# Kernel tuning notes

Measured on AMD Instinct MI355X. Metric: run time of the kernel, lower is better.

Reference implementation:

```python
import jax, jax.numpy as jnp
import numpy as np

DIM = 320
HEADS = 8
D_HEAD = 40
CTX_DIM = 768
INNER_FF = 4 * DIM  # 1280
EPS = 1e-5


def _ln(x, w, b):
    mu = jnp.mean(x, axis=-1, keepdims=True)
    var = jnp.mean(jnp.square(x - mu), axis=-1, keepdims=True)
    return (x - mu) * jax.lax.rsqrt(var + EPS) * w + b


def _attn(xq, ctx, Wq, Wk, Wv, Wo, bo):
    # Wq: [dim, inner]; Wk/Wv: [ctx_dim, inner]; Wo: [inner, dim]
    b, n, _ = xq.shape
    m = ctx.shape[1]
    scale = D_HEAD ** -0.5
    q = (xq @ Wq).reshape(b, n, HEADS, D_HEAD)
    k = (ctx @ Wk).reshape(b, m, HEADS, D_HEAD)
    v = (ctx @ Wv).reshape(b, m, HEADS, D_HEAD)
    sim = jnp.einsum('bihd,bjhd->bhij', q, k) * scale
    attn = jax.nn.softmax(sim, axis=-1)
    out = jnp.einsum('bhij,bjhd->bihd', attn, v).reshape(b, n, HEADS * D_HEAD)
    return out @ Wo + bo


def setup_inputs() -> dict:
    key = jax.random.key(0)
    ks = jax.random.split(key, 20)
    s = 0.02
    inner = HEADS * D_HEAD  # 320
    d = {
        'x': jax.random.normal(ks[0], (2, 4096, DIM), jnp.float32),
        'context': jax.random.normal(ks[1], (2, 77, CTX_DIM), jnp.float32),
        # norm params
        'ln1_w': jnp.ones((DIM,)), 'ln1_b': jnp.zeros((DIM,)),
        'ln2_w': jnp.ones((DIM,)), 'ln2_b': jnp.zeros((DIM,)),
        'ln3_w': jnp.ones((DIM,)), 'ln3_b': jnp.zeros((DIM,)),
        # attn1 (self)
        'a1_Wq': jax.random.normal(ks[2], (DIM, inner)) * s,
        'a1_Wk': jax.random.normal(ks[3], (DIM, inner)) * s,
        'a1_Wv': jax.random.normal(ks[4], (DIM, inner)) * s,
        'a1_Wo': jax.random.normal(ks[5], (inner, DIM)) * s,
        'a1_bo': jnp.zeros((DIM,)),
        # attn2 (cross)
        'a2_Wq': jax.random.normal(ks[6], (DIM, inner)) * s,
        'a2_Wk': jax.random.normal(ks[7], (CTX_DIM, inner)) * s,
        'a2_Wv': jax.random.normal(ks[8], (CTX_DIM, inner)) * s,
        'a2_Wo': jax.random.normal(ks[9], (inner, DIM)) * s,
        'a2_bo': jnp.zeros((DIM,)),
        # GEGLU feed-forward
        'ff_W1': jax.random.normal(ks[10], (DIM, 2 * INNER_FF)) * s,
        'ff_b1': jnp.zeros((2 * INNER_FF,)),
        'ff_W2': jax.random.normal(ks[11], (INNER_FF, DIM)) * s,
        'ff_b2': jnp.zeros((DIM,)),
    }
    return d


def reference(x, context, ln1_w, ln1_b, ln2_w, ln2_b, ln3_w, ln3_b,
              a1_Wq, a1_Wk, a1_Wv, a1_Wo, a1_bo,
              a2_Wq, a2_Wk, a2_Wv, a2_Wo, a2_bo,
              ff_W1, ff_b1, ff_W2, ff_b2):
    h = _ln(x, ln1_w, ln1_b)
    x = _attn(h, h, a1_Wq, a1_Wk, a1_Wv, a1_Wo, a1_bo) + x
    h = _ln(x, ln2_w, ln2_b)
    x = _attn(h, context, a2_Wq, a2_Wk, a2_Wv, a2_Wo, a2_bo) + x
    h = _ln(x, ln3_w, ln3_b)
    proj = h @ ff_W1 + ff_b1
    u, gate = jnp.split(proj, 2, axis=-1)
    ff = (u * jax.nn.gelu(gate, approximate=False)) @ ff_W2 + ff_b2
    return ff + x
```

## Files before the change

### kernel.cpp

```cpp
#include <hip/hip_runtime.h>
#include <hip/hip_bf16.h>
#include <math.h>

typedef __hip_bfloat16 bf16;
typedef __attribute__((ext_vector_type(8))) short bf16x8;
typedef __attribute__((ext_vector_type(4))) short bf16x4;
typedef __attribute__((ext_vector_type(4))) float f32x4;
typedef __attribute__((ext_vector_type(2))) unsigned int u32x2;

#define DIM 320
#define HEADS 8
#define DHEAD 40
#define CTXD 768
#define FFI 1280
#define NQ 4096
#define NCTX 77
#define BATCH 2

static __device__ __forceinline__ short f2bs(float v) {
    union { bf16 b; short s; } x; x.b = __float2bfloat16(v); return x.s;
}
static __device__ __forceinline__ float bs2f(short s) {
    return __uint_as_float(((unsigned)(unsigned short)s) << 16);
}
static __device__ __forceinline__ unsigned pkbf(float hi, float lo) {
    return __builtin_amdgcn_perm(__float_as_uint(hi), __float_as_uint(lo), 0x07060302u);
}

__global__ void __launch_bounds__(256) wtrans_all(
    const float* q1s, const float* k1s, const float* v1s, const float* o1s,
    const float* q2s, const float* o2s, const float* k2s, const float* v2s,
    const float* w1s, const float* w2s,
    short* q1d, short* k1d, short* v1d, short* o1d,
    short* q2d, short* o2d, short* k2d, short* v2d,
    short* w1d, short* w2d)
{
    int bid = blockIdx.x;
    const float* W; short* Wt; int K, N, base;
    if (bid < 600) {
        int ws = bid / 100; base = bid % 100; K = DIM; N = DIM;
        W  = ws == 0 ? q1s : ws == 1 ? k1s : ws == 2 ? v1s : ws == 3 ? o1s : ws == 4 ? q2s : o2s;
        Wt = ws == 0 ? q1d : ws == 1 ? k1d : ws == 2 ? v1d : ws == 3 ? o1d : ws == 4 ? q2d : o2d;
    } else if (bid < 1080) {
        int i = bid - 600; int ws = i / 240; base = i % 240; K = CTXD; N = DIM;
        W = ws ? v2s : k2s; Wt = ws ? v2d : k2d;
    } else if (bid < 1880) {
        base = bid - 1080; K = DIM; N = 2 * FFI; W = w1s; Wt = w1d;
    } else {
        base = bid - 1880; K = FFI; N = DIM; W = w2s; Wt = w2d;
    }
    int ntx = N / 32;
    int n0 = (base % ntx) * 32, k0 = (base / ntx) * 32;
    __shared__ float T[32][33];
    int c = threadIdx.x & 31, r8 = threadIdx.x >> 5;
#pragma unroll
    for (int rr = 0; rr < 4; ++rr) {
        int r = r8 + rr * 8;
        T[r][c] = W[(size_t)(k0 + r) * N + n0 + c];
    }
    __syncthreads();
#pragma unroll
    for (int rr = 0; rr < 4; ++rr) {
        int r = r8 + rr * 8;
        Wt[(size_t)(n0 + r) * K + k0 + c] = f2bs(T[c][r]);
    }
}

template<bool SRCB16>
__global__ void __launch_bounds__(256) ln_kernel(const void* __restrict__ srcp,
                          const float* __restrict__ w, const float* __restrict__ bp,
                          short* __restrict__ out, int rows)
{
    int row = blockIdx.x * 4 + (threadIdx.x >> 6);
    int lane = threadIdx.x & 63;
    float v[8];
    float s = 0.f, s2 = 0.f;
    if (lane < 40) {
        if (SRCB16) {
            bf16x8 xv = *(const bf16x8*)((const short*)srcp + (size_t)row * DIM + lane * 8);
#pragma unroll
            for (int j = 0; j < 8; ++j) { v[j] = bs2f(xv[j]); s += v[j]; s2 += v[j] * v[j]; }
        } else {
            const float* rp = (const float*)srcp + (size_t)row * DIM + lane * 8;
#pragma unroll
            for (int j = 0; j < 8; ++j) { v[j] = rp[j]; s += v[j]; s2 += v[j] * v[j]; }
        }
    }
#pragma unroll
    for (int off = 32; off; off >>= 1) { s += __shfl_xor(s, off); s2 += __shfl_xor(s2, off); }
    float mean = s * (1.f / DIM);
    float var = s2 * (1.f / DIM) - mean * mean;
    float rstd = rsqrtf(var + 1e-5f);
    if (lane < 40) {
        bf16x8 ov;
#pragma unroll
        for (int j = 0; j < 8; ++j)
            ov[j] = f2bs((v[j] - mean) * rstd * w[lane * 8 + j] + bp[lane * 8 + j]);
        *(bf16x8*)(out + (size_t)row * DIM + lane * 8) = ov;
    }
}

template<int MODE>
__global__ void __launch_bounds__(256) gemm128(const short* __restrict__ A,
                          const short* __restrict__ Wt,
                          const float* __restrict__ bias,
                          const float* __restrict__ res,
                          short* __restrict__ resb,
                          short* __restrict__ outb,
                          float* __restrict__ outf,
                          int N, int K, float oscale)
{
    __shared__ short As[128 * 72];
    __shared__ short Bs[64 * 72];
    const int tid = threadIdx.x;
    const int w = tid >> 6, lane = tid & 63, lrow = lane & 15, lgrp = lane >> 4;
    const int wr = w >> 1, wc = w & 1;
    const int m0 = blockIdx.y * 128, n0 = blockIdx.x * 64;
    f32x4 acc[4][2] = {};
    for (int k0 = 0; k0 < K; k0 += 64) {
        __syncthreads();
#pragma unroll
        for (int l = 0; l < 4; ++l) {
            int idx = tid + (l << 8);
            int arow = idx >> 3, ac = idx & 7;
            *(bf16x8*)&As[arow * 72 + ac * 8] =
                *(const bf16x8*)(A + (size_t)(m0 + arow) * K + k0 + ac * 8);
        }
#pragma unroll
        for (int l = 0; l < 2; ++l) {
            int idx = tid + (l << 8);
            int brow = idx >> 3, bc = idx & 7;
            *(bf16x8*)&Bs[brow * 72 + bc * 8] =
                *(const bf16x8*)(Wt + (size_t)(n0 + brow) * K + k0 + bc * 8);
        }
        __syncthreads();
#pragma unroll
        for (int s = 0; s < 2; ++s) {
            bf16x8 b0 = *(const bf16x8*)&Bs[(wc * 32 + lrow) * 72 + s * 32 + lgrp * 8];
            bf16x8 b1 = *(const bf16x8*)&Bs[(wc * 32 + 16 + lrow) * 72 + s * 32 + lgrp * 8];
#pragma unroll
            for (int m = 0; m < 4; ++m) {
                bf16x8 a = *(const bf16x8*)&As[(wr * 64 + m * 16 + lrow) * 72 + s * 32 + lgrp * 8];
                acc[m][0] = __builtin_amdgcn_mfma_f32_16x16x32_bf16(a, b0, acc[m][0], 0, 0, 0);
                acc[m][1] = __builtin_amdgcn_mfma_f32_16x16x32_bf16(a, b1, acc[m][1], 0, 0, 0);
            }
        }
    }
#pragma unroll
    for (int n = 0; n < 2; ++n) {
        int col = n0 + wc * 32 + n * 16 + lrow;
        float bvx = bias ? bias[col] : 0.f;
#pragma unroll
        for (int m = 0; m < 4; ++m) {
#pragma unroll
            for (int r = 0; r < 4; ++r) {
                int row = m0 + wr * 64 + m * 16 + lgrp * 4 + r;
                float v = acc[m][n][r] + bvx;
                size_t o = (size_t)row * N + col;
                if (MODE == 0)      outb[o] = f2bs(v * oscale);
                else if (MODE == 1) resb[o] = f2bs(v + res[o]);
                else if (MODE == 2) resb[o] = f2bs(v + bs2f(resb[o]));
                else                outf[o] = v + bs2f(resb[o]);
            }
        }
    }
}

__global__ void __launch_bounds__(256) qkv128(const short* __restrict__ A,
                          const short* __restrict__ wq, const short* __restrict__ wk,
                          const short* __restrict__ wv,
                          short* __restrict__ qb, short* __restrict__ kbuf,
                          short* __restrict__ vts, float qscale)
{
    __shared__ short As[128 * 72];
    __shared__ short Bs[64 * 72];
    const int tid = threadIdx.x;
    const int z = blockIdx.z;
    const short* Wt = z == 0 ? wq : z == 1 ? wk : wv;
    const int w = tid >> 6, lane = tid & 63, lrow = lane & 15, lgrp = lane >> 4;
    const int wr = w >> 1, wc = w & 1;
    const int m0 = blockIdx.y * 128, n0 = blockIdx.x * 64;
    f32x4 acc[4][2] = {};
    for (int k0 = 0; k0 < DIM; k0 += 64) {
        __syncthreads();
#pragma unroll
        for (int l = 0; l < 4; ++l) {
            int idx = tid + (l << 8);
            int arow = idx >> 3, ac = idx & 7;
            *(bf16x8*)&As[arow * 72 + ac * 8] =
                *(const bf16x8*)(A + (size_t)(m0 + arow) * DIM + k0 + ac * 8);
        }
#pragma unroll
        for (int l = 0; l < 2; ++l) {
            int idx = tid + (l << 8);
            int brow = idx >> 3, bc = idx & 7;
            *(bf16x8*)&Bs[brow * 72 + bc * 8] =
                *(const bf16x8*)(Wt + (size_t)(n0 + brow) * DIM + k0 + bc * 8);
        }
        __syncthreads();
#pragma unroll
        for (int s = 0; s < 2; ++s) {
            bf16x8 b0 = *(const bf16x8*)&Bs[(wc * 32 + lrow) * 72 + s * 32 + lgrp * 8];
            bf16x8 b1 = *(const bf16x8*)&Bs[(wc * 32 + 16 + lrow) * 72 + s * 32 + lgrp * 8];
#pragma unroll
            for (int m = 0; m < 4; ++m) {
                bf16x8 a = *(const bf16x8*)&As[(wr * 64 + m * 16 + lrow) * 72 + s * 32 + lgrp * 8];
                acc[m][0] = __builtin_amdgcn_mfma_f32_16x16x32_bf16(a, b0, acc[m][0], 0, 0, 0);
                acc[m][1] = __builtin_amdgcn_mfma_f32_16x16x32_bf16(a, b1, acc[m][1], 0, 0, 0);
            }
        }
    }
#pragma unroll
    for (int n = 0; n < 2; ++n) {
        int col = n0 + wc * 32 + n * 16 + lrow;
#pragma unroll
        for (int m = 0; m < 4; ++m) {
            if (z == 2) {
                int row0 = m0 + wr * 64 + m * 16 + lgrp * 4;
                int b_ = row0 >> 12, kv = row0 & (NQ - 1);
                int hh = col / DHEAD, d = col - hh * DHEAD;
                bf16x4 pv;
#pragma unroll
                for (int r = 0; r < 4; ++r) pv[r] = f2bs(acc[m][n][r]);
                *(bf16x4*)(vts + (size_t)((b_ * HEADS + hh) * 48 + d) * NQ + kv) = pv;
            } else {
#pragma unroll
                for (int r = 0; r < 4; ++r) {
                    int row = m0 + wr * 64 + m * 16 + lgrp * 4 + r;
                    float v = acc[m][n][r];
                    if (z == 0) qb[(size_t)row * DIM + col] = f2bs(v * qscale);
                    else        kbuf[(size_t)row * DIM + col] = f2bs(v);
                }
            }
        }
    }
}

__global__ void __launch_bounds__(256) mfma_crosskv(const float* __restrict__ ctx,
                          const short* __restrict__ wk2, const short* __restrict__ wv2,
                          short* __restrict__ k2, short* __restrict__ vt2)
{
    __shared__ short As[64 * 72];
    __shared__ short Bs[64 * 72];
    const int tid = threadIdx.x;
    const int z = blockIdx.z;
    const short* Wt = z ? wv2 : wk2;
    const int Mc = BATCH * NCTX;
    const int w = tid >> 6, lane = tid & 63, lrow = lane & 15, lgrp = lane >> 4;
    const int m0 = blockIdx.y * 64, n0 = blockIdx.x * 64;
    f32x4 acc[4] = {};
    for (int kb = 0; kb < CTXD / 64; ++kb) {
        const int k0 = kb << 6;
        __syncthreads();
#pragma unroll
        for (int l = 0; l < 2; ++l) {
            int idx = tid + (l << 8);
            int arow = idx >> 3, ac = idx & 7;
            int grow = m0 + arow;
            bf16x8 v = {};
            if (grow < Mc) {
                const float* Af = ctx + (size_t)grow * CTXD + k0 + ac * 8;
#pragma unroll
                for (int j = 0; j < 8; ++j) v[j] = f2bs(Af[j]);
            }
            *(bf16x8*)&As[arow * 72 + ac * 8] = v;
            *(bf16x8*)&Bs[arow * 72 + ac * 8] =
                *(const bf16x8*)(Wt + (size_t)(n0 + arow) * CTXD + k0 + ac * 8);
        }
        __syncthreads();
#pragma unroll
        for (int s = 0; s < 2; ++s) {
            bf16x8 a = *(const bf16x8*)&As[(w * 16 + lrow) * 72 + s * 32 + lgrp * 8];
#pragma unroll
            for (int ct = 0; ct < 4; ++ct) {
                bf16x8 b = *(const bf16x8*)&Bs[(ct * 16 + lrow) * 72 + s * 32 + lgrp * 8];
                acc[ct] = __builtin_amdgcn_mfma_f32_16x16x32_bf16(a, b, acc[ct], 0, 0, 0);
            }
        }
    }
#pragma unroll
    for (int ct = 0; ct < 4; ++ct) {
        int col = n0 + ct * 16 + lrow;
#pragma unroll
        for (int r = 0; r < 4; ++r) {
            int row = m0 + w * 16 + lgrp * 4 + r;
            if (row >= Mc) continue;
            float v = acc[ct][r];
            if (z == 0) k2[(size_t)row * DIM + col] = f2bs(v);
            else {
                int b_ = row / NCTX, kv = row - b_ * NCTX;
                int hh = col / DHEAD, d = col - hh * DHEAD;
                vt2[(size_t)((b_ * HEADS + hh) * 48 + d) * 128 + kv] = f2bs(v);
            }
        }
    }
}

__global__ void __launch_bounds__(256) geglu128(const short* __restrict__ A,
                           const short* __restrict__ Wt1,
                           const float* __restrict__ b1, short* __restrict__ G)
{
    __shared__ short As[128 * 72];
    __shared__ short Bu[64 * 72];
    __shared__ short Bg[64 * 72];
    const int tid = threadIdx.x;
    const int w = tid >> 6, lane = tid & 63, lrow = lane & 15, lgrp = lane >> 4;
    const int wr = w >> 1, wc = w & 1;
    const int m0 = blockIdx.y * 128, n0 = blockIdx.x * 64;
    f32x4 au[4][2] = {}, ag[4][2] = {};
    for (int k0 = 0; k0 < DIM; k0 += 64) {
        __syncthreads();
#pragma unroll
        for (int l = 0; l < 4; ++l) {
            int idx = tid + (l << 8);
            int arow = idx >> 3, ac = idx & 7;
            *(bf16x8*)&As[arow * 72 + ac * 8] =
                *(const bf16x8*)(A + (size_t)(m0 + arow) * DIM + k0 + ac * 8);
        }
#pragma unroll
        for (int l = 0; l < 2; ++l) {
            int idx = tid + (l << 8);
            int brow = idx >> 3, bc = idx & 7;
            *(bf16x8*)&Bu[brow * 72 + bc * 8] =
                *(const bf16x8*)(Wt1 + (size_t)(n0 + brow) * DIM + k0 + bc * 8);
            *(bf16x8*)&Bg[brow * 72 + bc * 8] =
                *(const bf16x8*)(Wt1 + (size_t)(FFI + n0 + brow) * DIM + k0 + bc * 8);
        }
        __syncthreads();
#pragma unroll
        for (int s = 0; s < 2; ++s) {
            bf16x8 bu0 = *(const bf16x8*)&Bu[(wc * 32 + lrow) * 72 + s * 32 + lgrp * 8];
            bf16x8 bu1 = *(const bf16x8*)&Bu[(wc * 32 + 16 + lrow) * 72 + s * 32 + lgrp * 8];
            bf16x8 bg0 = *(const bf16x8*)&Bg[(wc * 32 + lrow) * 72 + s * 32 + lgrp * 8];
            bf16x8 bg1 = *(const bf16x8*)&Bg[(wc * 32 + 16 + lrow) * 72 + s * 32 + lgrp * 8];
#pragma unroll
            for (int m = 0; m < 4; ++m) {
                bf16x8 a = *(const bf16x8*)&As[(wr * 64 + m * 16 + lrow) * 72 + s * 32 + lgrp * 8];
                au[m][0] = __builtin_amdgcn_mfma_f32_16x16x32_bf16(a, bu0, au[m][0], 0, 0, 0);
                au[m][1] = __builtin_amdgcn_mfma_f32_16x16x32_bf16(a, bu1, au[m][1], 0, 0, 0);
                ag[m][0] = __builtin_amdgcn_mfma_f32_16x16x32_bf16(a, bg0, ag[m][0], 0, 0, 0);
                ag[m][1] = __builtin_amdgcn_mfma_f32_16x16x32_bf16(a, bg1, ag[m][1], 0, 0, 0);
            }
        }
    }
#pragma unroll
    for (int n = 0; n < 2; ++n) {
        int col = n0 + wc * 32 + n * 16 + lrow;
        float bu = b1[col], bg = b1[FFI + col];
#pragma unroll
        for (int m = 0; m < 4; ++m) {
#pragma unroll
            for (int r = 0; r < 4; ++r) {
                int row = m0 + wr * 64 + m * 16 + lgrp * 4 + r;
                float u = au[m][n][r] + bu;
                float g = ag[m][n][r] + bg;
                float gelu = 0.5f * g * (1.f + erff(g * 0.70710678f));
                G[(size_t)row * FFI + col] = f2bs(u * gelu);
            }
        }
    }
}

template<bool FULL>
__global__ void __launch_bounds__(256) flash_mfma(const short* __restrict__ Q,
                           const short* __restrict__ Kb,
                           const short* __restrict__ VtG,
                           short* __restrict__ O,
                           int kvlen, int kvs)
{
    __shared__ short Ks[2][64 * 64];
    __shared__ short Vt[3][48 * 64];
    __shared__ short Ps[2][128 * 64];
    const int tid = threadIdx.x;
    const int w = tid >> 6, lane = tid & 63, lrow = lane & 15, lgrp = lane >> 4;
    const int hh = blockIdx.y, b = blockIdx.z;
    const int q0 = blockIdx.x * 128;
    const int swz = (lrow & 7) << 4;

    for (int i = tid; i < 1024; i += 256) ((bf16x8*)Ks)[i] = (bf16x8){};
    for (int i = tid; i < 1152; i += 256) {
        short fill = (((i % 384) >> 3) == 40) ? (short)0x3F80 : (short)0;
        bf16x8 f8 = {fill, fill, fill, fill, fill, fill, fill, fill};
        ((bf16x8*)Vt)[i] = f8;
    }

    const size_t qra = (size_t)(b * NQ + q0 + w * 32 + lrow) * DIM + hh * DHEAD;
    const size_t qrb = qra + (size_t)16 * DIM;
    bf16x8 bq0a = *(const bf16x8*)(Q + qra + lgrp * 8);
    bf16x8 bq0b = *(const bf16x8*)(Q + qrb + lgrp * 8);
    bf16x8 bq1a = {}, bq1b = {};
    if (lgrp == 0) {
        bq1a = *(const bf16x8*)(Q + qra + 32);
        bq1b = *(const bf16x8*)(Q + qrb + 32);
    }

    const int kv0 = tid / 5, cc0 = tid % 5;
    const bool isK1 = tid < 64;
    const int kv1 = (256 + tid) / 5, cc1 = (256 + tid) % 5;
    const int vd1 = (tid - 64) >> 3, vcc1 = (tid - 64) & 7;
    const bool hasV2 = tid < 128;
    const int vd2 = (192 + tid) >> 3, vcc2 = (192 + tid) & 7;

    const size_t kbase = (size_t)b * kvlen;
    const size_t vbase = (size_t)((b * HEADS + hh) * 48);

    const short* kp0 = Kb + (kbase + kv0) * DIM + hh * DHEAD + cc0 * 8;
    const short* kp1 = Kb + (kbase + (isK1 ? kv1 : 0)) * DIM + hh * DHEAD + (isK1 ? cc1 : 0) * 8;
    const short* vp1 = VtG + (vbase + (isK1 ? 0 : vd1)) * kvs + (isK1 ? 0 : vcc1) * 8;
    const short* vp2 = VtG + (vbase + (hasV2 ? vd2 : 0)) * kvs + (hasV2 ? vcc2 : 0) * 8;

    const int koff0 = kv0 * 128 + ((cc0 * 16) ^ ((kv0 & 7) << 4));
    const int koff1 = kv1 * 128 + ((cc1 * 16) ^ ((kv1 & 7) << 4));
    const int voff1 = vd1 * 128 + ((vcc1 * 16) ^ ((vd1 & 7) << 4));
    const int voff2 = vd2 * 128 + ((vcc2 * 16) ^ ((vd2 & 7) << 4));

    bf16x8 st0, st1, st2;
    auto issue = [&]() {
        st0 = *(const bf16x8*)kp0; kp0 += 64 * DIM;
        if (isK1) { st1 = *(const bf16x8*)kp1; kp1 += 64 * DIM; }
        else      { st1 = *(const bf16x8*)vp1; vp1 += 64; }
        if (hasV2) { st2 = *(const bf16x8*)vp2; vp2 += 64; }
    };
    auto commit = [&](char* kb_, char* vb_) {
        *(bf16x8*)(kb_ + koff0) = st0;
        if (isK1)  *(bf16x8*)(kb_ + koff1) = st1;
        else       *(bf16x8*)(vb_ + voff1) = st1;
        if (hasV2) *(bf16x8*)(vb_ + voff2) = st2;
    };

    f32x4 oa[3] = {}, ob[3] = {};

    char* kcur = (char*)Ks[0];
    char* knxt = (char*)Ks[1];
    char* vprev = (char*)Vt[2];
    char* vcur  = (char*)Vt[0];
    char* vnxt  = (char*)Vt[1];
    const int prow_off = (w * 32 + lrow) * 128;
    char* pcur  = (char*)Ps[0] + prow_off;
    char* pprev = (char*)Ps[1] + prow_off;

    auto pv_step = [&](char* vb_, char* pb_) {
        __builtin_amdgcn_s_setprio(1);
#pragma unroll
        for (int s = 0; s < 2; ++s) {
            bf16x8 bpa = *(const bf16x8*)(pb_ + ((s * 64 + lgrp * 16) ^ swz));
            bf16x8 bpb = *(const bf16x8*)(pb_ + 2048 + ((s * 64 + lgrp * 16) ^ swz));
#pragma unroll
            for (int dt = 0; dt < 3; ++dt) {
                bf16x8 av = *(const bf16x8*)(vb_ + (dt * 16 + lrow) * 128 + ((s * 64 + lgrp * 16) ^ swz));
                oa[dt] = __builtin_amdgcn_mfma_f32_16x16x32_bf16(av, bpa, oa[dt], 0, 0, 0);
                ob[dt] = __builtin_amdgcn_mfma_f32_16x16x32_bf16(av, bpb, ob[dt], 0, 0, 0);
            }
        }
        __builtin_amdgcn_s_setprio(0);
    };

    issue();
    __syncthreads();
    commit(kcur, vcur);
    issue();

    const int ntiles = (kvlen + 63) >> 6;
    for (int t = 0; t < ntiles; ++t) {
        __syncthreads();
        commit(knxt, vnxt);
        issue();

        if (t > 0) pv_step(vprev, pprev);

        f32x4 sa[4] = {}, sb[4] = {};
        __builtin_amdgcn_s_setprio(1);
#pragma unroll
        for (int ct = 0; ct < 4; ++ct) {
            const char* krow = kcur + (ct * 16 + lrow) * 128;
            bf16x8 ak0 = *(const bf16x8*)(krow + ((lgrp * 16) ^ swz));
            bf16x8 ak1 = *(const bf16x8*)(krow + ((64 + lgrp * 16) ^ swz));
            sa[ct] = __builtin_amdgcn_mfma_f32_16x16x32_bf16(ak0, bq0a, sa[ct], 0, 0, 0);
            sb[ct] = __builtin_amdgcn_mfma_f32_16x16x32_bf16(ak0, bq0b, sb[ct], 0, 0, 0);
            sa[ct] = __builtin_amdgcn_mfma_f32_16x16x32_bf16(ak1, bq1a, sa[ct], 0, 0, 0);
            sb[ct] = __builtin_amdgcn_mfma_f32_16x16x32_bf16(ak1, bq1b, sb[ct], 0, 0, 0);
        }
        __builtin_amdgcn_s_setprio(0);
        if (!FULL && (t << 6) + 64 > kvlen) {
#pragma unroll
            for (int ct = 0; ct < 4; ++ct)
#pragma unroll
                for (int r = 0; r < 4; ++r)
                    if ((t << 6) + ct * 16 + lgrp * 4 + r >= kvlen) { sa[ct][r] = -1e30f; sb[ct][r] = -1e30f; }
        }
#pragma unroll
        for (int ct = 0; ct < 4; ++ct) {
            float a0 = __builtin_amdgcn_exp2f(sa[ct][0]);
            float a1 = __builtin_amdgcn_exp2f(sa[ct][1]);
            float a2 = __builtin_amdgcn_exp2f(sa[ct][2]);
            float a3 = __builtin_amdgcn_exp2f(sa[ct][3]);
            u32x2 pka; pka[0] = pkbf(a1, a0); pka[1] = pkbf(a3, a2);
            *(u32x2*)(pcur + ((ct * 32 + lgrp * 8) ^ swz)) = pka;
            float b0 = __builtin_amdgcn_exp2f(sb[ct][0]);
            float b1 = __builtin_amdgcn_exp2f(sb[ct][1]);
            float b2 = __builtin_amdgcn_exp2f(sb[ct][2]);
            float b3 = __builtin_amdgcn_exp2f(sb[ct][3]);
            u32x2 pkb; pkb[0] = pkbf(b1, b0); pkb[1] = pkbf(b3, b2);
            *(u32x2*)(pcur + 2048 + ((ct * 32 + lgrp * 8) ^ swz)) = pkb;
        }
        { char* tk = kcur; kcur = knxt; knxt = tk; }
        { char* tv = vprev; vprev = vcur; vcur = vnxt; vnxt = tv; }
        { char* tp = pprev; pprev = pcur; pcur = tp; }
    }
    pv_step(vprev, pprev);

    float la = __shfl(oa[2][0], 32 + lrow);
    float lb = __shfl(ob[2][0], 32 + lrow);
    float ia = 1.f / la, ib = 1.f / lb;
#pragma unroll
    for (int dt = 0; dt < 3; ++dt) {
        int dbase = dt * 16 + lgrp * 4;
        if (dbase < DHEAD) {
            u32x2 ova, ovb;
            ova[0] = pkbf(oa[dt][1] * ia, oa[dt][0] * ia);
            ova[1] = pkbf(oa[dt][3] * ia, oa[dt][2] * ia);
            *(u32x2*)(O + qra + dbase) = ova;
            ovb[0] = pkbf(ob[dt][1] * ib, ob[dt][0] * ib);
            ovb[1] = pkbf(ob[dt][3] * ib, ob[dt][2] * ib);
            *(u32x2*)(O + qrb + dbase) = ovb;
        }
    }
}

extern "C" void kernel_launch(void* const* d_in, const int* in_sizes, int n_in,
                              void* d_out, int out_size, void* d_ws, size_t ws_size,
                              hipStream_t stream)
{
    const float* x      = (const float*)d_in[0];
    const float* ctx    = (const float*)d_in[1];
    const float* ln1_w  = (const float*)d_in[2];
    const float* ln1_b  = (const float*)d_in[3];
    const float* ln2_w  = (const float*)d_in[4];
    const float* ln2_b  = (const float*)d_in[5];
    const float* ln3_w  = (const float*)d_in[6];
    const float* ln3_b  = (const float*)d_in[7];
    const float* a1_Wq  = (const float*)d_in[8];
    const float* a1_Wk  = (const float*)d_in[9];
    const float* a1_Wv  = (const float*)d_in[10];
    const float* a1_Wo  = (const float*)d_in[11];
    const float* a1_bo  = (const float*)d_in[12];
    const float* a2_Wq  = (const float*)d_in[13];
    const float* a2_Wk  = (const float*)d_in[14];
    const float* a2_Wv  = (const float*)d_in[15];
    const float* a2_Wo  = (const float*)d_in[16];
    const float* a2_bo  = (const float*)d_in[17];
    const float* ff_W1  = (const float*)d_in[18];
    const float* ff_b1  = (const float*)d_in[19];
    const float* ff_W2  = (const float*)d_in[20];
    const float* ff_b2  = (const float*)d_in[21];

    const int M = BATCH * NQ;
    const float qscale2 = (float)(0.15811388300841898 * 1.4426950408889634);

    char* p = (char*)d_ws;
    auto carve = [&](size_t bytes) { char* r = p; p += (bytes + 255) & ~255ULL; return r; };
    short* h       = (short*)carve((size_t)M * DIM * 2);
    short* qb      = (short*)carve((size_t)M * DIM * 2);
    short* kbuf    = (short*)carve((size_t)M * DIM * 2);
    short* attnout = (short*)carve((size_t)M * DIM * 2);
    short* resb    = (short*)carve((size_t)M * DIM * 2);
    short* gbuf    = (short*)carve((size_t)M * FFI * 2);
    short* VtS     = (short*)carve((size_t)BATCH * HEADS * 48 * NQ * 2);
    short* Vt2     = (short*)carve((size_t)BATCH * HEADS * 48 * 128 * 2);
    short* k2      = (short*)carve((size_t)512 * DIM * 2);
    short* wtq1    = (short*)carve((size_t)DIM * DIM * 2);
    short* wtk1    = (short*)carve((size_t)DIM * DIM * 2);
    short* wtv1    = (short*)carve((size_t)DIM * DIM * 2);
    short* wto1    = (short*)carve((size_t)DIM * DIM * 2);
    short* wtq2    = (short*)carve((size_t)DIM * DIM * 2);
    short* wto2    = (short*)carve((size_t)DIM * DIM * 2);
    short* wtk2    = (short*)carve((size_t)DIM * CTXD * 2);
    short* wtv2    = (short*)carve((size_t)DIM * CTXD * 2);
    short* wt1     = (short*)carve((size_t)2 * FFI * DIM * 2);
    short* wt2     = (short*)carve((size_t)DIM * FFI * 2);

    dim3 blk(256);
    dim3 g128(DIM / 64, M / 128);
    dim3 gattn(NQ / 128, HEADS, BATCH);

    wtrans_all<<<2280, blk, 0, stream>>>(a1_Wq, a1_Wk, a1_Wv, a1_Wo, a2_Wq, a2_Wo,
                                         a2_Wk, a2_Wv, ff_W1, ff_W2,
                                         wtq1, wtk1, wtv1, wto1, wtq2, wto2,
                                         wtk2, wtv2, wt1, wt2);
    ln_kernel<false><<<M / 4, blk, 0, stream>>>(x, ln1_w, ln1_b, h, M);
    qkv128<<<dim3(5, 64, 3), blk, 0, stream>>>(h, wtq1, wtk1, wtv1, qb, kbuf, VtS, qscale2);
    flash_mfma<true><<<gattn, blk, 0, stream>>>(qb, kbuf, VtS, attnout, NQ, NQ);
    gemm128<1><<<g128, blk, 0, stream>>>(attnout, wto1, a1_bo, x, resb, nullptr, nullptr, DIM, DIM, 1.f);
    ln_kernel<true><<<M / 4, blk, 0, stream>>>(resb, ln2_w, ln2_b, h, M);
    gemm128<0><<<g128, blk, 0, stream>>>(h, wtq2, nullptr, nullptr, nullptr, qb, nullptr, DIM, DIM, qscale2);
    mfma_crosskv<<<dim3(5, 3, 2), blk, 0, stream>>>(ctx, wtk2, wtv2, k2, Vt2);
    flash_mfma<false><<<gattn, blk, 0, stream>>>(qb, k2, Vt2, attnout, NCTX, 128);
    gemm128<2><<<g128, blk, 0, stream>>>(attnout, wto2, a2_bo, nullptr, resb, nullptr, nullptr, DIM, DIM, 1.f);
    ln_kernel<true><<<M / 4, blk, 0, stream>>>(resb, ln3_w, ln3_b, h, M);
    geglu128<<<dim3(FFI / 64, M / 128), blk, 0, stream>>>(h, wt1, ff_b1, gbuf);
    gemm128<3><<<g128, blk, 0, stream>>>(gbuf, wt2, ff_b2, nullptr, resb, nullptr, (float*)d_out, DIM, FFI, 1.f);
}
```

Before: 232.5 us.

## Merge launches: fuse weight prep with LN1, cross Q with KV, single P buffer

New measurement: 221.1 us, median of 2. 4.9% less time.

```diff
diff --git a/kernel.cpp b/kernel.cpp
--- a/kernel.cpp
+++ b/kernel.cpp
@@ -27,64 +27,82 @@
     return __builtin_amdgcn_perm(__float_as_uint(hi), __float_as_uint(lo), 0x07060302u);
 }
 
-__global__ void __launch_bounds__(256) wtrans_all(
+__global__ void __launch_bounds__(256) prep_kernel(
     const float* q1s, const float* k1s, const float* v1s, const float* o1s,
     const float* q2s, const float* o2s, const float* k2s, const float* v2s,
     const float* w1s, const float* w2s,
     short* q1d, short* k1d, short* v1d, short* o1d,
     short* q2d, short* o2d, short* k2d, short* v2d,
-    short* w1d, short* w2d)
+    short* w1d, short* w2d,
+    const float* x, const float* ln1w, const float* ln1b, short* h)
 {
     int bid = blockIdx.x;
-    const float* W; short* Wt; int K, N, base;
-    if (bid < 600) {
-        int ws = bid / 100; base = bid % 100; K = DIM; N = DIM;
-        W  = ws == 0 ? q1s : ws == 1 ? k1s : ws == 2 ? v1s : ws == 3 ? o1s : ws == 4 ? q2s : o2s;
-        Wt = ws == 0 ? q1d : ws == 1 ? k1d : ws == 2 ? v1d : ws == 3 ? o1d : ws == 4 ? q2d : o2d;
-    } else if (bid < 1080) {
-        int i = bid - 600; int ws = i / 240; base = i % 240; K = CTXD; N = DIM;
-        W = ws ? v2s : k2s; Wt = ws ? v2d : k2d;
-    } else if (bid < 1880) {
-        base = bid - 1080; K = DIM; N = 2 * FFI; W = w1s; Wt = w1d;
+    if (bid < 2280) {
+        const float* W; short* Wt; int K, N, base;
+        if (bid < 600) {
+            int ws = bid / 100; base = bid % 100; K = DIM; N = DIM;
+            W  = ws == 0 ? q1s : ws == 1 ? k1s : ws == 2 ? v1s : ws == 3 ? o1s : ws == 4 ? q2s : o2s;
+            Wt = ws == 0 ? q1d : ws == 1 ? k1d : ws == 2 ? v1d : ws == 3 ? o1d : ws == 4 ? q2d : o2d;
+        } else if (bid < 1080) {
+            int i = bid - 600; int ws = i / 240; base = i % 240; K = CTXD; N = DIM;
+            W = ws ? v2s : k2s; Wt = ws ? v2d : k2d;
+        } else if (bid < 1880) {
+            base = bid - 1080; K = DIM; N = 2 * FFI; W = w1s; Wt = w1d;
+        } else {
+            base = bid - 1880; K = FFI; N = DIM; W = w2s; Wt = w2d;
+        }
+        int ntx = N / 32;
+        int n0 = (base % ntx) * 32, k0 = (base / ntx) * 32;
+        __shared__ float T[32][33];
+        int c = threadIdx.x & 31, r8 = threadIdx.x >> 5;
+#pragma unroll
+        for (int rr = 0; rr < 4; ++rr) {
+            int r = r8 + rr * 8;
+            T[r][c] = W[(size_t)(k0 + r) * N + n0 + c];
+        }
+        __syncthreads();
+#pragma unroll
+        for (int rr = 0; rr < 4; ++rr) {
+            int r = r8 + rr * 8;
+            Wt[(size_t)(n0 + r) * K + k0 + c] = f2bs(T[c][r]);
+        }
     } else {
-        base = bid - 1880; K = FFI; N = DIM; W = w2s; Wt = w2d;
-    }
-    int ntx = N / 32;
-    int n0 = (base % ntx) * 32, k0 = (base / ntx) * 32;
-    __shared__ float T[32][33];
-    int c = threadIdx.x & 31, r8 = threadIdx.x >> 5;
-#pragma unroll
-    for (int rr = 0; rr < 4; ++rr) {
-        int r = r8 + rr * 8;
-        T[r][c] = W[(size_t)(k0 + r) * N + n0 + c];
-    }
-    __syncthreads();
-#pragma unroll
-    for (int rr = 0; rr < 4; ++rr) {
-        int r = r8 + rr * 8;
-        Wt[(size_t)(n0 + r) * K + k0 + c] = f2bs(T[c][r]);
-    }
-}
-
-template<bool SRCB16>
-__global__ void __launch_bounds__(256) ln_kernel(const void* __restrict__ srcp,
+        int row = (bid - 2280) * 4 + (threadIdx.x >> 6);
+        int lane = threadIdx.x & 63;
+        float v[8];
+        float s = 0.f, s2 = 0.f;
+        if (lane < 40) {
+            const float* rp = x + (size_t)row * DIM + lane * 8;
+#pragma unroll
+            for (int j = 0; j < 8; ++j) { v[j] = rp[j]; s += v[j]; s2 += v[j] * v[j]; }
+        }
+#pragma unroll
+        for (int off = 32; off; off >>= 1) { s += __shfl_xor(s, off); s2 += __shfl_xor(s2, off); }
+        float mean = s * (1.f / DIM);
+        float var = s2 * (1.f / DIM) - mean * mean;
+        float rstd = rsqrtf(var + 1e-5f);
+        if (lane < 40) {
+            bf16x8 ov;
+#pragma unroll
+            for (int j = 0; j < 8; ++j)
+                ov[j] = f2bs((v[j] - mean) * rstd * ln1w[lane * 8 + j] + ln1b[lane * 8 + j]);
+            *(bf16x8*)(h + (size_t)row * DIM + lane * 8) = ov;
+        }
+    }
+}
+
+__global__ void __launch_bounds__(256) ln_b16(const short* __restrict__ srcp,
                           const float* __restrict__ w, const float* __restrict__ bp,
-                          short* __restrict__ out, int rows)
+                          short* __restrict__ out)
 {
     int row = blockIdx.x * 4 + (threadIdx.x >> 6);
     int lane = threadIdx.x & 63;
     float v[8];
     float s = 0.f, s2 = 0.f;
     if (lane < 40) {
-        if (SRCB16) {
-            bf16x8 xv = *(const bf16x8*)((const short*)srcp + (size_t)row * DIM + lane * 8);
-#pragma unroll
-            for (int j = 0; j < 8; ++j) { v[j] = bs2f(xv[j]); s += v[j]; s2 += v[j] * v[j]; }
-        } else {
-            const float* rp = (const float*)srcp + (size_t)row * DIM + lane * 8;
-#pragma unroll
-            for (int j = 0; j < 8; ++j) { v[j] = rp[j]; s += v[j]; s2 += v[j] * v[j]; }
-        }
+        bf16x8 xv = *(const bf16x8*)(srcp + (size_t)row * DIM + lane * 8);
+#pragma unroll
+        for (int j = 0; j < 8; ++j) { v[j] = bs2f(xv[j]); s += v[j]; s2 += v[j] * v[j]; }
     }
 #pragma unroll
     for (int off = 32; off; off >>= 1) { s += __shfl_xor(s, off); s2 += __shfl_xor(s2, off); }
@@ -236,61 +254,112 @@
     }
 }
 
-__global__ void __launch_bounds__(256) mfma_crosskv(const float* __restrict__ ctx,
+__global__ void __launch_bounds__(256) crossq_kv(const short* __restrict__ h,
+                          const short* __restrict__ wq2,
+                          const float* __restrict__ ctx,
                           const short* __restrict__ wk2, const short* __restrict__ wv2,
-                          short* __restrict__ k2, short* __restrict__ vt2)
-{
-    __shared__ short As[64 * 72];
+                          short* __restrict__ qb, short* __restrict__ k2,
+                          short* __restrict__ vt2, float qscale)
+{
+    __shared__ short As[128 * 72];
     __shared__ short Bs[64 * 72];
     const int tid = threadIdx.x;
-    const int z = blockIdx.z;
-    const short* Wt = z ? wv2 : wk2;
-    const int Mc = BATCH * NCTX;
     const int w = tid >> 6, lane = tid & 63, lrow = lane & 15, lgrp = lane >> 4;
-    const int m0 = blockIdx.y * 64, n0 = blockIdx.x * 64;
-    f32x4 acc[4] = {};
-    for (int kb = 0; kb < CTXD / 64; ++kb) {
-        const int k0 = kb << 6;
-        __syncthreads();
-#pragma unroll
-        for (int l = 0; l < 2; ++l) {
-            int idx = tid + (l << 8);
-            int arow = idx >> 3, ac = idx & 7;
-            int grow = m0 + arow;
-            bf16x8 v = {};
-            if (grow < Mc) {
-                const float* Af = ctx + (size_t)grow * CTXD + k0 + ac * 8;
-#pragma unroll
-                for (int j = 0; j < 8; ++j) v[j] = f2bs(Af[j]);
-            }
-            *(bf16x8*)&As[arow * 72 + ac * 8] = v;
-            *(bf16x8*)&Bs[arow * 72 + ac * 8] =
-                *(const bf16x8*)(Wt + (size_t)(n0 + arow) * CTXD + k0 + ac * 8);
-        }
-        __syncthreads();
-#pragma unroll
-        for (int s = 0; s < 2; ++s) {
-            bf16x8 a = *(const bf16x8*)&As[(w * 16 + lrow) * 72 + s * 32 + lgrp * 8];
-#pragma unroll
-            for (int ct = 0; ct < 4; ++ct) {
-                bf16x8 b = *(const bf16x8*)&Bs[(ct * 16 + lrow) * 72 + s * 32 + lgrp * 8];
-                acc[ct] = __builtin_amdgcn_mfma_f32_16x16x32_bf16(a, b, acc[ct], 0, 0, 0);
-            }
-        }
-    }
-#pragma unroll
-    for (int ct = 0; ct < 4; ++ct) {
-        int col = n0 + ct * 16 + lrow;
-#pragma unroll
-        for (int r = 0; r < 4; ++r) {
-            int row = m0 + w * 16 + lgrp * 4 + r;
-            if (row >= Mc) continue;
-            float v = acc[ct][r];
-            if (z == 0) k2[(size_t)row * DIM + col] = f2bs(v);
-            else {
-                int b_ = row / NCTX, kv = row - b_ * NCTX;
-                int hh = col / DHEAD, d = col - hh * DHEAD;
-                vt2[(size_t)((b_ * HEADS + hh) * 48 + d) * 128 + kv] = f2bs(v);
+    int bid = blockIdx.x;
+    if (bid < 320) {
+        const int wr = w >> 1, wc = w & 1;
+        const int m0 = (bid / 5) * 128, n0 = (bid % 5) * 64;
+        f32x4 acc[4][2] = {};
+        for (int k0 = 0; k0 < DIM; k0 += 64) {
+            __syncthreads();
+#pragma unroll
+            for (int l = 0; l < 4; ++l) {
+                int idx = tid + (l << 8);
+                int arow = idx >> 3, ac = idx & 7;
+                *(bf16x8*)&As[arow * 72 + ac * 8] =
+                    *(const bf16x8*)(h + (size_t)(m0 + arow) * DIM + k0 + ac * 8);
+            }
+#pragma unroll
+            for (int l = 0; l < 2; ++l) {
+                int idx = tid + (l << 8);
+                int brow = idx >> 3, bc = idx & 7;
+                *(bf16x8*)&Bs[brow * 72 + bc * 8] =
+                    *(const bf16x8*)(wq2 + (size_t)(n0 + brow) * DIM + k0 + bc * 8);
+            }
+            __syncthreads();
+#pragma unroll
+            for (int s = 0; s < 2; ++s) {
+                bf16x8 b0 = *(const bf16x8*)&Bs[(wc * 32 + lrow) * 72 + s * 32 + lgrp * 8];
+                bf16x8 b1 = *(const bf16x8*)&Bs[(wc * 32 + 16 + lrow) * 72 + s * 32 + lgrp * 8];
+#pragma unroll
+                for (int m = 0; m < 4; ++m) {
+                    bf16x8 a = *(const bf16x8*)&As[(wr * 64 + m * 16 + lrow) * 72 + s * 32 + lgrp * 8];
+                    acc[m][0] = __builtin_amdgcn_mfma_f32_16x16x32_bf16(a, b0, acc[m][0], 0, 0, 0);
+                    acc[m][1] = __builtin_amdgcn_mfma_f32_16x16x32_bf16(a, b1, acc[m][1], 0, 0, 0);
+                }
+            }
+        }
+#pragma unroll
+        for (int n = 0; n < 2; ++n) {
+            int col = n0 + wc * 32 + n * 16 + lrow;
+#pragma unroll
+            for (int m = 0; m < 4; ++m)
+#pragma unroll
+                for (int r = 0; r < 4; ++r) {
+                    int row = m0 + wr * 64 + m * 16 + lgrp * 4 + r;
+                    qb[(size_t)row * DIM + col] = f2bs(acc[m][n][r] * qscale);
+                }
+        }
+    } else {
+        int i = bid - 320;
+        int z = i / 15, r_ = i % 15;
+        const short* Wt = z ? wv2 : wk2;
+        const int Mc = BATCH * NCTX;
+        const int m0 = (r_ / 5) * 64, n0 = (r_ % 5) * 64;
+        f32x4 acc[4] = {};
+        for (int kb = 0; kb < CTXD / 64; ++kb) {
+            const int k0 = kb << 6;
+            __syncthreads();
+#pragma unroll
+            for (int l = 0; l < 2; ++l) {
+                int idx = tid + (l << 8);
+                int arow = idx >> 3, ac = idx & 7;
+                int grow = m0 + arow;
+                bf16x8 v = {};
+                if (grow < Mc) {
+                    const float* Af = ctx + (size_t)grow * CTXD + k0 + ac * 8;
+#pragma unroll
+                    for (int j = 0; j < 8; ++j) v[j] = f2bs(Af[j]);
+                }
+                *(bf16x8*)&As[arow * 72 + ac * 8] = v;
+                *(bf16x8*)&Bs[arow * 72 + ac * 8] =
+                    *(const bf16x8*)(Wt + (size_t)(n0 + arow) * CTXD + k0 + ac * 8);
+            }
+            __syncthreads();
+#pragma unroll
+            for (int s = 0; s < 2; ++s) {
+                bf16x8 a = *(const bf16x8*)&As[(w * 16 + lrow) * 72 + s * 32 + lgrp * 8];
+#pragma unroll
+                for (int ct = 0; ct < 4; ++ct) {
+                    bf16x8 b = *(const bf16x8*)&Bs[(ct * 16 + lrow) * 72 + s * 32 + lgrp * 8];
+                    acc[ct] = __builtin_amdgcn_mfma_f32_16x16x32_bf16(a, b, acc[ct], 0, 0, 0);
+                }
+            }
+        }
+#pragma unroll
+        for (int ct = 0; ct < 4; ++ct) {
+            int col = n0 + ct * 16 + lrow;
+            int hh = col / DHEAD, d = col - hh * DHEAD;
+#pragma unroll
+            for (int r = 0; r < 4; ++r) {
+                int row = m0 + w * 16 + lgrp * 4 + r;
+                if (row >= Mc) continue;
+                float v = acc[ct][r];
+                if (z == 0) k2[(size_t)row * DIM + col] = f2bs(v);
+                else {
+                    int b_ = row / NCTX, kv = row - b_ * NCTX;
+                    vt2[(size_t)((b_ * HEADS + hh) * 48 + d) * 128 + kv] = f2bs(v);
+                }
             }
         }
     }
@@ -370,7 +439,7 @@
 {
     __shared__ short Ks[2][64 * 64];
     __shared__ short Vt[3][48 * 64];
-    __shared__ short Ps[2][128 * 64];
+    __shared__ short Ps[128 * 64];
     const int tid = threadIdx.x;
     const int w = tid >> 6, lane = tid & 63, lrow = lane & 15, lgrp = lane >> 4;
     const int hh = blockIdx.y, b = blockIdx.z;
@@ -435,16 +504,14 @@
     char* vprev = (char*)Vt[2];
     char* vcur  = (char*)Vt[0];
     char* vnxt  = (char*)Vt[1];
-    const int prow_off = (w * 32 + lrow) * 128;
-    char* pcur  = (char*)Ps[0] + prow_off;
-    char* pprev = (char*)Ps[1] + prow_off;
-
-    auto pv_step = [&](char* vb_, char* pb_) {
+    char* pp = (char*)Ps + (w * 32 + lrow) * 128;
+
+    auto pv_step = [&](char* vb_) {
         __builtin_amdgcn_s_setprio(1);
 #pragma unroll
         for (int s = 0; s < 2; ++s) {
-            bf16x8 bpa = *(const bf16x8*)(pb_ + ((s * 64 + lgrp * 16) ^ swz));
-            bf16x8 bpb = *(const bf16x8*)(pb_ + 2048 + ((s * 64 + lgrp * 16) ^ swz));
+            bf16x8 bpa = *(const bf16x8*)(pp + ((s * 64 + lgrp * 16) ^ swz));
+            bf16x8 bpb = *(const bf16x8*)(pp + 2048 + ((s * 64 + lgrp * 16) ^ swz));
 #pragma unroll
             for (int dt = 0; dt < 3; ++dt) {
                 bf16x8 av = *(const bf16x8*)(vb_ + (dt * 16 + lrow) * 128 + ((s * 64 + lgrp * 16) ^ swz));
@@ -466,7 +533,7 @@
         commit(knxt, vnxt);
         issue();
 
-        if (t > 0) pv_step(vprev, pprev);
+        if (t > 0) pv_step(vprev);
 
         f32x4 sa[4] = {}, sb[4] = {};
         __builtin_amdgcn_s_setprio(1);
@@ -495,19 +562,18 @@
             float a2 = __builtin_amdgcn_exp2f(sa[ct][2]);
             float a3 = __builtin_amdgcn_exp2f(sa[ct][3]);
             u32x2 pka; pka[0] = pkbf(a1, a0); pka[1] = pkbf(a3, a2);
-            *(u32x2*)(pcur + ((ct * 32 + lgrp * 8) ^ swz)) = pka;
+            *(u32x2*)(pp + ((ct * 32 + lgrp * 8) ^ swz)) = pka;
             float b0 = __builtin_amdgcn_exp2f(sb[ct][0]);
             float b1 = __builtin_amdgcn_exp2f(sb[ct][1]);
             float b2 = __builtin_amdgcn_exp2f(sb[ct][2]);
             float b3 = __builtin_amdgcn_exp2f(sb[ct][3]);
             u32x2 pkb; pkb[0] = pkbf(b1, b0); pkb[1] = pkbf(b3, b2);
-            *(u32x2*)(pcur + 2048 + ((ct * 32 + lgrp * 8) ^ swz)) = pkb;
+            *(u32x2*)(pp + 2048 + ((ct * 32 + lgrp * 8) ^ swz)) = pkb;
         }
         { char* tk = kcur; kcur = knxt; knxt = tk; }
         { char* tv = vprev; vprev = vcur; vcur = vnxt; vnxt = tv; }
-        { char* tp = pprev; pprev = pcur; pcur = tp; }
-    }
-    pv_step(vprev, pprev);
+    }
+    pv_step(vprev);
 
     float la = __shfl(oa[2][0], 32 + lrow);
     float lb = __shfl(ob[2][0], 32 + lrow);
@@ -583,20 +649,18 @@
     dim3 g128(DIM / 64, M / 128);
     dim3 gattn(NQ / 128, HEADS, BATCH);
 
-    wtrans_all<<<2280, blk, 0, stream>>>(a1_Wq, a1_Wk, a1_Wv, a1_Wo, a2_Wq, a2_Wo,
-                                         a2_Wk, a2_Wv, ff_W1, ff_W2,
-                                         wtq1, wtk1, wtv1, wto1, wtq2, wto2,
-                                         wtk2, wtv2, wt1, wt2);
-    ln_kernel<false><<<M / 4, blk, 0, stream>>>(x, ln1_w, ln1_b, h, M);
+    prep_kernel<<<2280 + M / 4, blk, 0, stream>>>(
+        a1_Wq, a1_Wk, a1_Wv, a1_Wo, a2_Wq, a2_Wo, a2_Wk, a2_Wv, ff_W1, ff_W2,
+        wtq1, wtk1, wtv1, wto1, wtq2, wto2, wtk2, wtv2, wt1, wt2,
+        x, ln1_w, ln1_b, h);
     qkv128<<<dim3(5, 64, 3), blk, 0, stream>>>(h, wtq1, wtk1, wtv1, qb, kbuf, VtS, qscale2);
     flash_mfma<true><<<gattn, blk, 0, stream>>>(qb, kbuf, VtS, attnout, NQ, NQ);
     gemm128<1><<<g128, blk, 0, stream>>>(attnout, wto1, a1_bo, x, resb, nullptr, nullptr, DIM, DIM, 1.f);
-    ln_kernel<true><<<M / 4, blk, 0, stream>>>(resb, ln2_w, ln2_b, h, M);
-    gemm128<0><<<g128, blk, 0, stream>>>(h, wtq2, nullptr, nullptr, nullptr, qb, nullptr, DIM, DIM, qscale2);
-    mfma_crosskv<<<dim3(5, 3, 2), blk, 0, stream>>>(ctx, wtk2, wtv2, k2, Vt2);
+    ln_b16<<<M / 4, blk, 0, stream>>>(resb, ln2_w, ln2_b, h);
+    crossq_kv<<<350, blk, 0, stream>>>(h, wtq2, ctx, wtk2, wtv2, qb, k2, Vt2, qscale2);
     flash_mfma<false><<<gattn, blk, 0, stream>>>(qb, k2, Vt2, attnout, NCTX, 128);
     gemm128<2><<<g128, blk, 0, stream>>>(attnout, wto2, a2_bo, nullptr, resb, nullptr, nullptr, DIM, DIM, 1.f);
-    ln_kernel<true><<<M / 4, blk, 0, stream>>>(resb, ln3_w, ln3_b, h, M);
+    ln_b16<<<M / 4, blk, 0, stream>>>(resb, ln3_w, ln3_b, h);
     geglu128<<<dim3(FFI / 64, M / 128), blk, 0, stream>>>(h, wt1, ff_b1, gbuf);
     gemm128<3><<<g128, blk, 0, stream>>>(gbuf, wt2, ff_b2, nullptr, resb, nullptr, (float*)d_out, DIM, FFI, 1.f);
 }
```
